# Kernel optimization log

Measured on AMD Instinct MI355X. Metric: run time of the kernel, lower is better.

## Reference

```python
import jax, jax.numpy as jnp
import numpy as np

EPS = 1e-5

def setup_inputs() -> dict:
    key = jax.random.key(0)
    ks = jax.random.split(key, 9)
    N, D, L, C = 1, 128, 256, 256
    OC, PC = 32, 256
    msa_matrix = jax.random.normal(ks[0], (N, D, L, C), dtype=jnp.float32)
    ln_w = jnp.ones((C,), dtype=jnp.float32)
    ln_b = jnp.zeros((C,), dtype=jnp.float32)
    s = 1.0 / np.sqrt(C)
    Wl = jax.random.uniform(ks[1], (OC, C), dtype=jnp.float32, minval=-s, maxval=s)
    bl = jax.random.uniform(ks[2], (OC,), dtype=jnp.float32, minval=-s, maxval=s)
    Wr = jax.random.uniform(ks[3], (OC, C), dtype=jnp.float32, minval=-s, maxval=s)
    br = jax.random.uniform(ks[4], (OC,), dtype=jnp.float32, minval=-s, maxval=s)
    so = 1.0 / np.sqrt(OC * OC)
    Wout = jax.random.uniform(ks[5], (PC, OC * OC), dtype=jnp.float32, minval=-so, maxval=so)
    bout = jax.random.uniform(ks[6], (PC,), dtype=jnp.float32, minval=-so, maxval=so)
    return {"msa_matrix": msa_matrix, "ln_w": ln_w, "ln_b": ln_b,
            "Wl": Wl, "bl": bl, "Wr": Wr, "br": br, "Wout": Wout, "bout": bout}

def reference(msa_matrix, ln_w, ln_b, Wl, bl, Wr, br, Wout, bout):
    N, D, L, C = msa_matrix.shape
    OC = Wl.shape[0]
    # LayerNorm over channels
    mu = jnp.mean(msa_matrix, axis=-1, keepdims=True)
    var = jnp.var(msa_matrix, axis=-1, keepdims=True)
    x = (msa_matrix - mu) * jax.lax.rsqrt(var + EPS) * ln_w + ln_b
    # Dual projections: [N, D, L, OC]
    left = jnp.einsum('ndlc,oc->ndlo', x, Wl) + bl
    right = (jnp.einsum('ndlc,oc->ndlo', x, Wr) + br) / D
    # Outer-product mean over MSA depth: [N, L, L, OC, OC]
    outprod = jnp.einsum('ndlc,ndmq->nlmcq', left, right)
    outprod = outprod.reshape(N, L, L, OC * OC)
    # Output projection to pair channels
    return jnp.einsum('nlmk,pk->nlmp', outprod, Wout) + bout
```

## Files before the change

### kernel.cpp

```cpp
#include <hip/hip_runtime.h>

#define EPS 1e-5f

static constexpr int D  = 128;
static constexpr int L  = 256;
static constexpr int C  = 256;
static constexpr int OC = 32;
static constexpr int PC = 256;

typedef __attribute__((ext_vector_type(8))) short bfrag8;
typedef __attribute__((ext_vector_type(4))) short bhalf4;
typedef __attribute__((ext_vector_type(4))) float f32x4;
typedef __attribute__((ext_vector_type(4))) unsigned int u32x4;

__device__ inline unsigned short f2bf(float f) {
  union { float f; unsigned u; } v; v.f = f;
  unsigned r = v.u + 0x7FFF + ((v.u >> 16) & 1);
  return (unsigned short)(r >> 16);
}

__global__ __launch_bounds__(256, 4)
void prep_ln(const float* __restrict__ msa,
             const float* __restrict__ lnw, const float* __restrict__ lnb,
             const float* __restrict__ Wl, const float* __restrict__ Wr,
             const float* __restrict__ Wout,
             const float* __restrict__ bl, const float* __restrict__ br,
             unsigned short* __restrict__ Wbf3,
             unsigned short* __restrict__ leftT, unsigned short* __restrict__ rightT) {
  const int t = threadIdx.x;
  const int b = blockIdx.x;

  if (b < 64) {
    #pragma unroll
    for (int j2 = 0; j2 < 4; ++j2) {
      const int e0 = (b * 256 + t) * 16 + j2 * 4;
      const int lane = (e0 >> 3) & 63, ks = (e0 >> 9) & 31, pf = e0 >> 14;
      const int p = pf * 16 + (lane & 15);
      unsigned short v[4];
      #pragma unroll
      for (int j = 0; j < 4; ++j) {
        const int kp = ks * 32 + ((lane >> 4) * 8) + ((e0 + j) & 7);
        const int c = kp & 31, q = kp >> 5;
        v[j] = f2bf(Wout[p * 1024 + c * 32 + q]);
      }
      *(bhalf4*)(Wbf3 + e0) = *(bhalf4*)v;
    }
    return;
  }

  __shared__ char xb[32768];

  const int bb = b - 64;
  const int lane = t & 63, w = t >> 6;
  const int d0 = (bb & 15) * 8, l0 = (bb >> 4) * 8;

  float4 xv[16];
  #pragma unroll
  for (int i = 0; i < 16; ++i) {
    const int r = i * 4 + w, dd = r & 7, ll = r >> 3;
    xv[i] = *(const float4*)(msa + ((size_t)(d0 + dd) * 256 + (l0 + ll)) * 256 + lane * 4);
  }

  bfrag8 wf[8];
  {
    const int n = w * 16 + (lane & 15);
    const int side = n >> 5, o = n & 31;
    const float* Wrow = (side ? Wr : Wl) + o * 256 + ((lane >> 4) * 8);
    #pragma unroll
    for (int ks = 0; ks < 8; ++ks) {
      const float4 w0 = *(const float4*)(Wrow + ks * 32);
      const float4 w1 = *(const float4*)(Wrow + ks * 32 + 4);
      unsigned short u[8];
      u[0] = f2bf(w0.x); u[1] = f2bf(w0.y); u[2] = f2bf(w0.z); u[3] = f2bf(w0.w);
      u[4] = f2bf(w1.x); u[5] = f2bf(w1.y); u[6] = f2bf(w1.z); u[7] = f2bf(w1.w);
      wf[ks] = *(bfrag8*)u;
    }
  }

  float mu[16], rs[16];
  #pragma unroll
  for (int i = 0; i < 16; ++i) {
    float s  = xv[i].x + xv[i].y + xv[i].z + xv[i].w;
    float s2 = xv[i].x * xv[i].x + xv[i].y * xv[i].y + xv[i].z * xv[i].z + xv[i].w * xv[i].w;
    #pragma unroll
    for (int off = 32; off >= 1; off >>= 1) {
      s  += __shfl_xor(s, off);
      s2 += __shfl_xor(s2, off);
    }
    mu[i] = s * (1.0f / C);
    rs[i] = rsqrtf(s2 * (1.0f / C) - mu[i] * mu[i] + EPS);
  }

  {
    const float4 wv = *(const float4*)(lnw + lane * 4);
    const float4 bv = *(const float4*)(lnb + lane * 4);
    #pragma unroll
    for (int i = 0; i < 16; ++i) {
      const int r = i * 4 + w;
      float4 v = xv[i];
      unsigned short u[4];
      u[0] = f2bf((v.x - mu[i]) * rs[i] * wv.x + bv.x);
      u[1] = f2bf((v.y - mu[i]) * rs[i] * wv.y + bv.y);
      u[2] = f2bf((v.z - mu[i]) * rs[i] * wv.z + bv.z);
      u[3] = f2bf((v.w - mu[i]) * rs[i] * wv.w + bv.w);
      *(bhalf4*)&xb[r * 512 + ((lane * 8) ^ ((r & 7) << 4))] = *(bhalf4*)u;
    }
  }
  __syncthreads();

  f32x4 acc[4];
  #pragma unroll
  for (int mf = 0; mf < 4; ++mf) acc[mf] = (f32x4)0.f;
  #pragma unroll
  for (int ks = 0; ks < 8; ++ks) {
    #pragma unroll
    for (int mf = 0; mf < 4; ++mf) {
      const int row = mf * 16 + (lane & 15);
      const bfrag8 af = *(const bfrag8*)&xb[row * 512 +
                          ((ks * 64 + ((lane >> 4) << 4)) ^ ((row & 7) << 4))];
      acc[mf] = __builtin_amdgcn_mfma_f32_16x16x32_bf16(af, wf[ks], acc[mf], 0, 0, 0);
    }
  }

  {
    const int n = w * 16 + (lane & 15);
    const int side = n >> 5, o = n & 31;
    const float bias = side ? br[o] : bl[o];
    const float sc = side ? (1.0f / D) : 1.0f;
    unsigned short* dst = side ? rightT : leftT;
    #pragma unroll
    for (int mf = 0; mf < 4; ++mf) {
      const int rbase = mf * 16 + ((lane >> 4) << 2);
      const int ll = rbase >> 3, ddb = rbase & 7;
      unsigned short u[4];
      #pragma unroll
      for (int r = 0; r < 4; ++r) u[r] = f2bf((acc[mf][r] + bias) * sc);
      *(bhalf4*)(dst + ((size_t)(l0 + ll) * 32 + o) * 128 + d0 + ddb) = *(bhalf4*)u;
    }
  }
}

__global__ __launch_bounds__(512, 4)
void fused_mfma(const unsigned short* __restrict__ leftT,
                const unsigned short* __restrict__ rightT,
                const unsigned short* __restrict__ Wbf3,
                const float* __restrict__ bout,
                float* __restrict__ out) {
  __shared__ char smem[65536];

  const int flat = blockIdx.x;
  const int wg = (flat & 7) * 256 + (flat >> 3);
  const int mt = wg & 31, lt = wg >> 5;
  const int l0 = lt * 4, m0 = mt * 8;

  const char* Aslab = (const char*)(leftT  + (size_t)l0 * 32 * 128);
  const char* Bslab = (const char*)(rightT + (size_t)m0 * 32 * 128);

  const int tid = threadIdx.x, lane = tid & 63, w = tid >> 6;
  const int wr = w >> 2, wc = w & 3;

  f32x4 acc[4][4];
  #pragma unroll
  for (int i = 0; i < 4; ++i)
    #pragma unroll
    for (int j = 0; j < 4; ++j) acc[i][j] = (f32x4)0.f;

  auto stageA = [&](int kh, int dst) {
    #pragma unroll
    for (int i = 0; i < 2; ++i) {
      const int lb = (i * 512 + tid) * 16;
      const int row = lb >> 7;
      const int sb = (lb & 127) ^ ((row & 7) << 4);
      __builtin_amdgcn_global_load_lds((const void*)(Aslab + (size_t)row * 256 + kh * 128 + sb),
                                       (void*)&smem[dst + lb], 16, 0, 0);
    }
  };
  auto stageB = [&](int kh) {
    #pragma unroll
    for (int i = 0; i < 4; ++i) {
      const int lb = (i * 512 + tid) * 16;
      const int row = lb >> 7;
      const int sb = (lb & 127) ^ ((row & 7) << 4);
      __builtin_amdgcn_global_load_lds((const void*)(Bslab + (size_t)row * 256 + kh * 128 + sb),
                                       (void*)&smem[16384 + lb], 16, 0, 0);
    }
  };
  auto computeKh = [&](int abase) {
    #pragma unroll
    for (int ks = 0; ks < 2; ++ks) {
      const int kb = ks * 64 + ((lane >> 4) << 4);
      bfrag8 a[4], b[4];
      #pragma unroll
      for (int i = 0; i < 4; ++i) {
        const int row = wr * 64 + i * 16 + (lane & 15);
        a[i] = *(const bfrag8*)&smem[abase + (row << 7) + (kb ^ ((row & 7) << 4))];
      }
      #pragma unroll
      for (int j = 0; j < 4; ++j) {
        const int row = wc * 64 + j * 16 + (lane & 15);
        b[j] = *(const bfrag8*)&smem[16384 + (row << 7) + (kb ^ ((row & 7) << 4))];
      }
      #pragma unroll
      for (int i = 0; i < 4; ++i)
        #pragma unroll
        for (int j = 0; j < 4; ++j)
          acc[i][j] = __builtin_amdgcn_mfma_f32_16x16x32_bf16(a[i], b[j], acc[i][j], 0, 0, 0);
    }
  };

  stageA(0, 0);
  stageB(0);
  __syncthreads();
  stageA(1, 49152);
  u32x4 b1r[4];
  #pragma unroll
  for (int i = 0; i < 4; ++i) {
    const int lb = (i * 512 + tid) * 16;
    const int row = lb >> 7;
    const int sb = (lb & 127) ^ ((row & 7) << 4);
    b1r[i] = *(const u32x4*)(Bslab + (size_t)row * 256 + 128 + sb);
  }
  computeKh(0);
  __syncthreads();
  #pragma unroll
  for (int i = 0; i < 4; ++i)
    *(u32x4*)&smem[16384 + (i * 512 + tid) * 16] = b1r[i];
  __syncthreads();
  computeKh(49152);
  __syncthreads();

  {
    #pragma unroll
    for (int i = 0; i < 4; ++i) {
      const int rowb = wr * 64 + i * 16 + ((lane >> 4) << 2);
      const int ll = rowb >> 5, cc = rowb & 31;
      #pragma unroll
      for (int j = 0; j < 4; ++j) {
        const int col = wc * 64 + j * 16 + (lane & 15);
        const int mm = col >> 5, q = col & 31;
        const int pair = ll * 8 + mm;
        const int kp = q * 32 + cc;
        const int S = (pair & 7) ^ ((q >> 1) & 7);
        const int byte = pair * 2048 + ((kp * 2) ^ (S << 4));
        uint2 u;
        u.x = (unsigned)f2bf(acc[i][j][0]) | ((unsigned)f2bf(acc[i][j][1]) << 16);
        u.y = (unsigned)f2bf(acc[i][j][2]) | ((unsigned)f2bf(acc[i][j][3]) << 16);
        *(uint2*)&smem[byte] = u;
      }
    }
  }

  const unsigned short* wp0 = Wbf3 + (((size_t)(w * 2)     * 32) * 64 + lane) * 8;
  const unsigned short* wp1 = Wbf3 + (((size_t)(w * 2 + 1) * 32) * 64 + lane) * 8;

  bfrag8 wfs[4][2];
  #pragma unroll
  for (int s = 0; s < 4; ++s) {
    wfs[s][0] = *(const bfrag8*)(wp0 + s * 512);
    wfs[s][1] = *(const bfrag8*)(wp1 + s * 512);
  }
  __syncthreads();

  f32x4 oacc[2][2];
  #pragma unroll
  for (int u = 0; u < 2; ++u)
    #pragma unroll
    for (int pj = 0; pj < 2; ++pj) oacc[u][pj] = (f32x4)0.f;

  auto ldos = [&](int ks, bfrag8* o) {
    #pragma unroll
    for (int pj = 0; pj < 2; ++pj) {
      const int pair = pj * 16 + (lane & 15);
      const int S = (pair & 7) ^ ((ks >> 1) & 7);
      o[pj] = *(const bfrag8*)&smem[pair * 2048 + ((ks * 64 + ((lane >> 4) << 4)) ^ (S << 4))];
    }
  };

  bfrag8 osA[2], osB[2];
  ldos(0, osA);

  #pragma unroll
  for (int ks = 0; ks < 32; ks += 2) {
    ldos(ks + 1, osB);
    __builtin_amdgcn_s_setprio(1);
    oacc[0][0] = __builtin_amdgcn_mfma_f32_16x16x32_bf16(wfs[ks & 3][0], osA[0], oacc[0][0], 0, 0, 0);
    oacc[0][1] = __builtin_amdgcn_mfma_f32_16x16x32_bf16(wfs[ks & 3][0], osA[1], oacc[0][1], 0, 0, 0);
    oacc[1][0] = __builtin_amdgcn_mfma_f32_16x16x32_bf16(wfs[ks & 3][1], osA[0], oacc[1][0], 0, 0, 0);
    oacc[1][1] = __builtin_amdgcn_mfma_f32_16x16x32_bf16(wfs[ks & 3][1], osA[1], oacc[1][1], 0, 0, 0);
    __builtin_amdgcn_s_setprio(0);
    if (ks + 4 < 32) {
      wfs[ks & 3][0] = *(const bfrag8*)(wp0 + (ks + 4) * 512);
      wfs[ks & 3][1] = *(const bfrag8*)(wp1 + (ks + 4) * 512);
    }
    if (ks + 2 < 32) ldos(ks + 2, osA);
    __builtin_amdgcn_s_setprio(1);
    oacc[0][0] = __builtin_amdgcn_mfma_f32_16x16x32_bf16(wfs[(ks + 1) & 3][0], osB[0], oacc[0][0], 0, 0, 0);
    oacc[0][1] = __builtin_amdgcn_mfma_f32_16x16x32_bf16(wfs[(ks + 1) & 3][0], osB[1], oacc[0][1], 0, 0, 0);
    oacc[1][0] = __builtin_amdgcn_mfma_f32_16x16x32_bf16(wfs[(ks + 1) & 3][1], osB[0], oacc[1][0], 0, 0, 0);
    oacc[1][1] = __builtin_amdgcn_mfma_f32_16x16x32_bf16(wfs[(ks + 1) & 3][1], osB[1], oacc[1][1], 0, 0, 0);
    __builtin_amdgcn_s_setprio(0);
    if (ks + 5 < 32) {
      wfs[(ks + 1) & 3][0] = *(const bfrag8*)(wp0 + (ks + 5) * 512);
      wfs[(ks + 1) & 3][1] = *(const bfrag8*)(wp1 + (ks + 5) * 512);
    }
  }

  {
    #pragma unroll
    for (int u = 0; u < 2; ++u) {
      const int p0 = (w * 2 + u) * 16 + ((lane >> 4) << 2);
      const float4 bb = *(const float4*)&bout[p0];
      #pragma unroll
      for (int pj = 0; pj < 2; ++pj) {
        const int pair = pj * 16 + (lane & 15);
        const int ll = pair >> 3, mm = pair & 7;
        float4 v;
        v.x = oacc[u][pj][0] + bb.x;
        v.y = oacc[u][pj][1] + bb.y;
        v.z = oacc[u][pj][2] + bb.z;
        v.w = oacc[u][pj][3] + bb.w;
        *(float4*)&out[((size_t)(l0 + ll) * L + (m0 + mm)) * PC + p0] = v;
      }
    }
  }
}

extern "C" void kernel_launch(void* const* d_in, const int* in_sizes, int n_in,
                              void* d_out, int out_size, void* d_ws, size_t ws_size,
                              hipStream_t stream) {
  const float* msa  = (const float*)d_in[0];
  const float* ln_w = (const float*)d_in[1];
  const float* ln_b = (const float*)d_in[2];
  const float* Wl   = (const float*)d_in[3];
  const float* bl   = (const float*)d_in[4];
  const float* Wr   = (const float*)d_in[5];
  const float* br   = (const float*)d_in[6];
  const float* Wout = (const float*)d_in[7];
  const float* bout = (const float*)d_in[8];
  float* out = (float*)d_out;

  unsigned short* leftT  = (unsigned short*)d_ws;
  unsigned short* rightT = leftT + (size_t)L * 32 * 128;
  unsigned short* Wbf3   = rightT + (size_t)L * 32 * 128;

  prep_ln<<<dim3(576), 256, 0, stream>>>(msa, ln_w, ln_b, Wl, Wr, Wout, bl, br,
                                         Wbf3, leftT, rightT);
  fused_mfma<<<dim3(2048), 512, 0, stream>>>(leftT, rightT, Wbf3, bout, out);
}
```

Before: 83.29 us.

## Permute Wout K-order to allow 16-byte LDS stores and deepen LDS prefetch

The Wout bf16 reordering in the prep kernel now uses a permuted channel index within each 32-wide block. This lets the outer-product accumulators from two adjacent row tiles be packed into a single 16-byte LDS store instead of two 8-byte stores. The second-stage GEMM loop also changes from a two-buffer ping-pong to a four-deep rotating prefetch of LDS operand fragments. The aim is fewer LDS store instructions and more latency hiding, at the cost of extra registers and correctness that depends on the permutation matching on both sides.

```diff
diff --git a/kernel.cpp b/kernel.cpp
--- a/kernel.cpp
+++ b/kernel.cpp
@@ -40,8 +40,9 @@
       #pragma unroll
       for (int j = 0; j < 4; ++j) {
         const int kp = ks * 32 + ((lane >> 4) * 8) + ((e0 + j) & 7);
-        const int c = kp & 31, q = kp >> 5;
-        v[j] = f2bf(Wout[p * 1024 + c * 32 + q]);
+        const int q = kp >> 5, t5 = kp & 31;
+        const int cc = ((t5 >> 2) & 1) * 16 + (t5 >> 3) * 4 + (t5 & 3);
+        v[j] = f2bf(Wout[p * 1024 + cc * 32 + q]);
       }
       *(bhalf4*)(Wbf3 + e0) = *(bhalf4*)v;
     }
@@ -230,22 +231,23 @@
   __syncthreads();
 
   {
-    #pragma unroll
-    for (int i = 0; i < 4; ++i) {
-      const int rowb = wr * 64 + i * 16 + ((lane >> 4) << 2);
-      const int ll = rowb >> 5, cc = rowb & 31;
+    const int c2_16 = (lane >> 4) << 4;
+    #pragma unroll
+    for (int ip = 0; ip < 2; ++ip) {
+      const int ll = wr * 2 + ip;
       #pragma unroll
       for (int j = 0; j < 4; ++j) {
         const int col = wc * 64 + j * 16 + (lane & 15);
         const int mm = col >> 5, q = col & 31;
         const int pair = ll * 8 + mm;
-        const int kp = q * 32 + cc;
         const int S = (pair & 7) ^ ((q >> 1) & 7);
-        const int byte = pair * 2048 + ((kp * 2) ^ (S << 4));
-        uint2 u;
-        u.x = (unsigned)f2bf(acc[i][j][0]) | ((unsigned)f2bf(acc[i][j][1]) << 16);
-        u.y = (unsigned)f2bf(acc[i][j][2]) | ((unsigned)f2bf(acc[i][j][3]) << 16);
-        *(uint2*)&smem[byte] = u;
+        const int byte = pair * 2048 + ((q * 64 + c2_16) ^ (S << 4));
+        u32x4 u;
+        u[0] = (unsigned)f2bf(acc[2 * ip][j][0])     | ((unsigned)f2bf(acc[2 * ip][j][1]) << 16);
+        u[1] = (unsigned)f2bf(acc[2 * ip][j][2])     | ((unsigned)f2bf(acc[2 * ip][j][3]) << 16);
+        u[2] = (unsigned)f2bf(acc[2 * ip + 1][j][0]) | ((unsigned)f2bf(acc[2 * ip + 1][j][1]) << 16);
+        u[3] = (unsigned)f2bf(acc[2 * ip + 1][j][2]) | ((unsigned)f2bf(acc[2 * ip + 1][j][3]) << 16);
+        *(u32x4*)&smem[byte] = u;
       }
     }
   }
@@ -276,32 +278,23 @@
     }
   };
 
-  bfrag8 osA[2], osB[2];
-  ldos(0, osA);
-
-  #pragma unroll
-  for (int ks = 0; ks < 32; ks += 2) {
-    ldos(ks + 1, osB);
+  bfrag8 osf[4][2];
+  ldos(0, osf[0]);
+  ldos(1, osf[1]);
+  ldos(2, osf[2]);
+
+  #pragma unroll
+  for (int ks = 0; ks < 32; ++ks) {
+    if (ks + 3 < 32) ldos(ks + 3, osf[(ks + 3) & 3]);
     __builtin_amdgcn_s_setprio(1);
-    oacc[0][0] = __builtin_amdgcn_mfma_f32_16x16x32_bf16(wfs[ks & 3][0], osA[0], oacc[0][0], 0, 0, 0);
-    oacc[0][1] = __builtin_amdgcn_mfma_f32_16x16x32_bf16(wfs[ks & 3][0], osA[1], oacc[0][1], 0, 0, 0);
-    oacc[1][0] = __builtin_amdgcn_mfma_f32_16x16x32_bf16(wfs[ks & 3][1], osA[0], oacc[1][0], 0, 0, 0);
-    oacc[1][1] = __builtin_amdgcn_mfma_f32_16x16x32_bf16(wfs[ks & 3][1], osA[1], oacc[1][1], 0, 0, 0);
+    oacc[0][0] = __builtin_amdgcn_mfma_f32_16x16x32_bf16(wfs[ks & 3][0], osf[ks & 3][0], oacc[0][0], 0, 0, 0);
+    oacc[0][1] = __builtin_amdgcn_mfma_f32_16x16x32_bf16(wfs[ks & 3][0], osf[ks & 3][1], oacc[0][1], 0, 0, 0);
+    oacc[1][0] = __builtin_amdgcn_mfma_f32_16x16x32_bf16(wfs[ks & 3][1], osf[ks & 3][0], oacc[1][0], 0, 0, 0);
+    oacc[1][1] = __builtin_amdgcn_mfma_f32_16x16x32_bf16(wfs[ks & 3][1], osf[ks & 3][1], oacc[1][1], 0, 0, 0);
     __builtin_amdgcn_s_setprio(0);
     if (ks + 4 < 32) {
       wfs[ks & 3][0] = *(const bfrag8*)(wp0 + (ks + 4) * 512);
       wfs[ks & 3][1] = *(const bfrag8*)(wp1 + (ks + 4) * 512);
-    }
-    if (ks + 2 < 32) ldos(ks + 2, osA);
-    __builtin_amdgcn_s_setprio(1);
-    oacc[0][0] = __builtin_amdgcn_mfma_f32_16x16x32_bf16(wfs[(ks + 1) & 3][0], osB[0], oacc[0][0], 0, 0, 0);
-    oacc[0][1] = __builtin_amdgcn_mfma_f32_16x16x32_bf16(wfs[(ks + 1) & 3][0], osB[1], oacc[0][1], 0, 0, 0);
-    oacc[1][0] = __builtin_amdgcn_mfma_f32_16x16x32_bf16(wfs[(ks + 1) & 3][1], osB[0], oacc[1][0], 0, 0, 0);
-    oacc[1][1] = __builtin_amdgcn_mfma_f32_16x16x32_bf16(wfs[(ks + 1) & 3][1], osB[1], oacc[1][1], 0, 0, 0);
-    __builtin_amdgcn_s_setprio(0);
-    if (ks + 5 < 32) {
-      wfs[(ks + 1) & 3][0] = *(const bfrag8*)(wp0 + (ks + 5) * 512);
-      wfs[(ks + 1) & 3][1] = *(const bfrag8*)(wp1 + (ks + 5) * 512);
     }
   }
 
```

After: 81.82 us, median of 3. No clear change (-1.8%).
